# Kernel optimization log

Hardware: AMD Instinct MI355X
Metric: run time of the kernel (lower is better)

## Reference

```python
import jax, jax.numpy as jnp
import numpy as np

EPS = 1e-4
B, D, DOUT = 8192, 4096, 4096


def setup_inputs() -> dict:
    key = jax.random.key(0)
    k1, k2, k3 = jax.random.split(key, 3)
    x = jax.random.normal(k1, (B, D), dtype=jnp.float32)
    # Linear layer params (torch nn.Linear: y = x @ W.T + b)
    W = jax.random.normal(k2, (DOUT, D), dtype=jnp.float32) * (1.0 / np.sqrt(D))
    b = jax.random.normal(k3, (DOUT,), dtype=jnp.float32) * 0.01
    return {"x": x, "W": W, "b": b}


def reference(x, W, b):
    # hess = sum_b x[b] outer x[b] + eps*I  == X^T X + eps*I (a GEMM, not a
    # materialized [B,D,D] broadcast like the torch source)
    d = x.shape[1]
    hess = jnp.einsum('bi,bj->ij', x, x) + EPS * jnp.eye(d, dtype=x.dtype)
    out = x @ W.T + b  # wrapped nn.Linear
    return out, hess
```

## Files before the change

### kernel.cpp

```cpp
#include <hip/hip_runtime.h>
#include <hip/hip_bf16.h>

#define BDIM 8192
#define DDIM 4096
#define DOUTD 4096

typedef __attribute__((ext_vector_type(8))) short short8;
typedef __attribute__((ext_vector_type(16))) float floatx16;

__device__ inline unsigned short f32_to_bf16_rne(float f) {
    unsigned int u = __float_as_uint(f);
    unsigned int lsb = (u >> 16) & 1u;
    u += 0x7fffu + lsb;
    return (unsigned short)(u >> 16);
}

__device__ inline void gload_lds16(const void* g, void* lds) {
    __builtin_amdgcn_global_load_lds(
        (const __attribute__((address_space(1))) void*)g,
        (__attribute__((address_space(3))) void*)lds,
        16, 0, 0);
}

__global__ __launch_bounds__(256)
void convert_transpose_x(const float* __restrict__ x,
                         unsigned short* __restrict__ xb,
                         unsigned short* __restrict__ xT) {
    __shared__ __align__(8) unsigned short tile[64][66];
    const int t = threadIdx.x;
    const int tb = blockIdx.x * 64;
    const int td = blockIdx.y * 64;
#pragma unroll
    for (int p = 0; p < 4; ++p) {
        int c = t + p * 256;
        int row  = c >> 4;
        int col4 = (c & 15) << 2;
        float4 v = *(const float4*)&x[(size_t)(tb + row) * DDIM + td + col4];
        ushort4 o;
        o.x = f32_to_bf16_rne(v.x);
        o.y = f32_to_bf16_rne(v.y);
        o.z = f32_to_bf16_rne(v.z);
        o.w = f32_to_bf16_rne(v.w);
        *(ushort4*)&xb[(size_t)(tb + row) * DDIM + td + col4] = o;
        ushort2 lo; lo.x = o.x; lo.y = o.y;
        ushort2 hi2; hi2.x = o.z; hi2.y = o.w;
        *(ushort2*)&tile[row][col4]     = lo;
        *(ushort2*)&tile[row][col4 + 2] = hi2;
    }
    __syncthreads();
#pragma unroll
    for (int p = 0; p < 4; ++p) {
        int c = t + p * 256;
        int drow = c >> 4;
        int b4   = (c & 15) << 2;
        ushort4 o;
        o.x = tile[b4 + 0][drow];
        o.y = tile[b4 + 1][drow];
        o.z = tile[b4 + 2][drow];
        o.w = tile[b4 + 3][drow];
        *(ushort4*)&xT[(size_t)(td + drow) * BDIM + tb + b4] = o;
    }
}

__global__ __launch_bounds__(256)
void convert_w_kernel(const float* __restrict__ W, unsigned short* __restrict__ Wb) {
    size_t i = ((size_t)blockIdx.x * 256 + threadIdx.x) * 8;
    float4 a = *(const float4*)&W[i];
    float4 b = *(const float4*)&W[i + 4];
    short8 o;
    o[0] = (short)f32_to_bf16_rne(a.x);
    o[1] = (short)f32_to_bf16_rne(a.y);
    o[2] = (short)f32_to_bf16_rne(a.z);
    o[3] = (short)f32_to_bf16_rne(a.w);
    o[4] = (short)f32_to_bf16_rne(b.x);
    o[5] = (short)f32_to_bf16_rne(b.y);
    o[6] = (short)f32_to_bf16_rne(b.z);
    o[7] = (short)f32_to_bf16_rne(b.w);
    *(short8*)&Wb[i] = o;
}

#define CFENCE() asm volatile("" ::: "memory")
#define BAR() do { CFENCE(); __builtin_amdgcn_s_barrier(); CFENCE(); } while (0)
#define MFMA_BF16 __builtin_amdgcn_mfma_f32_32x32x16_bf16

template <bool HESS>
__global__ __launch_bounds__(512, 2)
void gemm256(const unsigned short* __restrict__ A,
             const unsigned short* __restrict__ B,
             const float* __restrict__ bias,
             float* __restrict__ C,
             int M, int N, int K) {
    __shared__ __align__(16) unsigned short As[32768];
    __shared__ __align__(16) unsigned short Bs[32768];

    const int t    = threadIdx.x;
    const int lane = t & 63;
    const int w    = t >> 6;
    const int lm   = lane & 31;
    const int hi   = lane >> 5;
    const int key2 = (lm >> 2) & 3;
    const int wm   = w >> 2;
    const int wn   = w & 3;
    const size_t bm = (size_t)blockIdx.y * 256;
    const size_t bn = (size_t)blockIdx.x * 256;
    const int NT = K >> 6;

    const int kh_w = w >> 2;
    const int wq   = w & 3;
    const int rsub = lane >> 2;
    const int csrc = (lane & 3) ^ ((lane >> 4) & 3);
    const unsigned short* gA0 = A + (bm + wq * 32 + rsub) * (size_t)K + kh_w * 32 + csrc * 8;
    const unsigned short* gB0 = B + (bn + wq * 32 + rsub) * (size_t)K + kh_w * 32 + csrc * 8;
    char* ldsA = (char*)As + kh_w * 16384 + wq * 2048;
    char* ldsB = (char*)Bs + kh_w * 16384 + wq * 2048;
    const size_t rowK16 = (size_t)16 * K;
    const size_t halfK  = (size_t)128 * K;

#define STAGE_A(tj, h, buf) do {                                   \
        const size_t _ko = (size_t)(tj) * 64 + (size_t)(h) * halfK;\
        char* _d = ldsA + (buf) * 32768 + (h) * 8192;              \
        gload_lds16(gA0 + _ko, _d);                                \
        gload_lds16(gA0 + _ko + rowK16, _d + 1024);                \
    } while (0)
#define STAGE_B(tj, h, buf) do {                                   \
        const size_t _ko = (size_t)(tj) * 64 + (size_t)(h) * halfK;\
        char* _d = ldsB + (buf) * 32768 + (h) * 8192;              \
        gload_lds16(gB0 + _ko, _d);                                \
        gload_lds16(gB0 + _ko + rowK16, _d + 1024);                \
    } while (0)

    const int AROWb = (wm * 128 + lm) * 32;
    const int BROWb = (wn * 32 + lm) * 32;
    int pos[4];
#pragma unroll
    for (int s = 0; s < 4; ++s)
        pos[s] = (s >> 1) * 8192 + ((((s & 1) * 2 + hi) ^ key2) * 8);

    floatx16 acc[4][2];
#pragma unroll
    for (int i = 0; i < 4; ++i)
#pragma unroll
        for (int j = 0; j < 2; ++j)
#pragma unroll
            for (int g = 0; g < 16; ++g)
                acc[i][j][g] = 0.f;

    short8 af0[2][4], af1[2][4], bf[2][4];

#define READS_EARLY(AB2) do {                                              \
        _Pragma("unroll")                                                  \
        for (int mi = 0; mi < 2; ++mi) {                                   \
            af0[mi][0] = *(const short8*)&As[(AB2) + AROWb + mi * 1024 + pos[0]]; \
            af0[mi][1] = *(const short8*)&As[(AB2) + AROWb + mi * 1024 + pos[1]]; \
        }                                                                  \
        bf[0][0] = *(const short8*)&Bs[(AB2) + BROWb + pos[0]];            \
        bf[0][1] = *(const short8*)&Bs[(AB2) + BROWb + pos[1]];            \
    } while (0)

#define TILE_BODY(J, BUFC) do {                                            \
        constexpr int AB  = (BUFC) * 16384;                                \
        constexpr int AB2 = ((BUFC) ^ 1) * 16384;                          \
         \
         \
        _Pragma("unroll")                                                  \
        for (int mi = 0; mi < 2; ++mi) {                                   \
            af0[mi][2] = *(const short8*)&As[AB + AROWb + mi * 1024 + pos[2]]; \
            af0[mi][3] = *(const short8*)&As[AB + AROWb + mi * 1024 + pos[3]]; \
        }                                                                  \
        bf[1][0] = *(const short8*)&Bs[AB + BROWb + 4096 + pos[0]];        \
        bf[1][1] = *(const short8*)&Bs[AB + BROWb + 4096 + pos[1]];        \
        if ((J) + 1 < NT) STAGE_B((J) + 1, 1, (BUFC) ^ 1);                 \
        BAR();                                                             \
        __builtin_amdgcn_s_setprio(1);                                     \
        _Pragma("unroll")                                                  \
        for (int s = 0; s < 2; ++s) {                                      \
            acc[0][0] = MFMA_BF16(af0[0][s], bf[0][s], acc[0][0], 0, 0, 0);\
            acc[1][0] = MFMA_BF16(af0[1][s], bf[0][s], acc[1][0], 0, 0, 0);\
            acc[0][1] = MFMA_BF16(af0[0][s], bf[1][s], acc[0][1], 0, 0, 0);\
            acc[1][1] = MFMA_BF16(af0[1][s], bf[1][s], acc[1][1], 0, 0, 0);\
        }                                                                  \
        __builtin_amdgcn_s_setprio(0);                                     \
        asm volatile("s_waitcnt lgkmcnt(0)" ::: "memory");                 \
        BAR();                                                             \
         \
         \
        bf[0][2] = *(const short8*)&Bs[AB + BROWb + pos[2]];               \
        bf[0][3] = *(const short8*)&Bs[AB + BROWb + pos[3]];               \
        bf[1][2] = *(const short8*)&Bs[AB + BROWb + 4096 + pos[2]];        \
        bf[1][3] = *(const short8*)&Bs[AB + BROWb + 4096 + pos[3]];        \
        _Pragma("unroll")                                                  \
        for (int mi = 0; mi < 2; ++mi) {                                   \
            af1[mi][0] = *(const short8*)&As[AB + AROWb + 2048 + mi * 1024 + pos[0]]; \
            af1[mi][1] = *(const short8*)&As[AB + AROWb + 2048 + mi * 1024 + pos[1]]; \
        }                                                                  \
        if ((J) + 2 < NT) STAGE_B((J) + 2, 0, (BUFC));                     \
        BAR();                                                             \
        __builtin_amdgcn_s_setprio(1);                                     \
        _Pragma("unroll")                                                  \
        for (int s = 2; s < 4; ++s) {                                      \
            acc[0][0] = MFMA_BF16(af0[0][s], bf[0][s], acc[0][0], 0, 0, 0);\
            acc[1][0] = MFMA_BF16(af0[1][s], bf[0][s], acc[1][0], 0, 0, 0);\
            acc[0][1] = MFMA_BF16(af0[0][s], bf[1][s], acc[0][1], 0, 0, 0);\
            acc[1][1] = MFMA_BF16(af0[1][s], bf[1][s], acc[1][1], 0, 0, 0);\
        }                                                                  \
        __builtin_amdgcn_s_setprio(0);                                     \
        asm volatile("s_waitcnt lgkmcnt(0)" ::: "memory");                 \
        BAR();                                                             \
         \
         \
        _Pragma("unroll")                                                  \
        for (int mi = 0; mi < 2; ++mi) {                                   \
            af1[mi][2] = *(const short8*)&As[AB + AROWb + 2048 + mi * 1024 + pos[2]]; \
            af1[mi][3] = *(const short8*)&As[AB + AROWb + 2048 + mi * 1024 + pos[3]]; \
        }                                                                  \
        if ((J) + 2 < NT) STAGE_A((J) + 2, 0, (BUFC));                     \
        BAR();                                                             \
        __builtin_amdgcn_s_setprio(1);                                     \
        _Pragma("unroll")                                                  \
        for (int s = 0; s < 2; ++s) {                                      \
            acc[2][0] = MFMA_BF16(af1[0][s], bf[0][s], acc[2][0], 0, 0, 0);\
            acc[3][0] = MFMA_BF16(af1[1][s], bf[0][s], acc[3][0], 0, 0, 0);\
            acc[2][1] = MFMA_BF16(af1[0][s], bf[1][s], acc[2][1], 0, 0, 0);\
            acc[3][1] = MFMA_BF16(af1[1][s], bf[1][s], acc[3][1], 0, 0, 0);\
        }                                                                  \
        __builtin_amdgcn_s_setprio(0);                                     \
        asm volatile("s_waitcnt lgkmcnt(0)" ::: "memory");                 \
        BAR();                                                             \
         \
         \
        if ((J) + 2 < NT) STAGE_A((J) + 2, 1, (BUFC));                     \
        if ((J) < NT - 2)       asm volatile("s_waitcnt vmcnt(6)" ::: "memory"); \
        else if ((J) == NT - 2) asm volatile("s_waitcnt vmcnt(0)" ::: "memory"); \
        BAR();                                                             \
        __builtin_amdgcn_s_setprio(1);                                     \
        _Pragma("unroll")                                                  \
        for (int s = 2; s < 4; ++s) {                                      \
            acc[2][0] = MFMA_BF16(af1[0][s], bf[0][s], acc[2][0], 0, 0, 0);\
            acc[3][0] = MFMA_BF16(af1[1][s], bf[0][s], acc[3][0], 0, 0, 0);\
            acc[2][1] = MFMA_BF16(af1[0][s], bf[1][s], acc[2][1], 0, 0, 0);\
            acc[3][1] = MFMA_BF16(af1[1][s], bf[1][s], acc[3][1], 0, 0, 0);\
        }                                                                  \
        __builtin_amdgcn_s_setprio(0);                                     \
        if ((J) + 1 < NT) READS_EARLY(AB2);                                \
        BAR();                                                             \
    } while (0)

    STAGE_B(0, 0, 0); STAGE_A(0, 0, 0); STAGE_B(0, 1, 0); STAGE_A(0, 1, 0);
    STAGE_B(1, 0, 1); STAGE_A(1, 0, 1); STAGE_A(1, 1, 1);
    asm volatile("s_waitcnt vmcnt(6)" ::: "memory");
    BAR();
    READS_EARLY(0);

    for (int jj = 0; jj < NT; jj += 2) {
        TILE_BODY(jj, 0);
        TILE_BODY(jj + 1, 1);
    }
#undef STAGE_A
#undef STAGE_B
#undef READS_EARLY
#undef TILE_BODY

    float bv[2];
#pragma unroll
    for (int n2 = 0; n2 < 2; ++n2)
        bv[n2] = HESS ? 0.f : bias[bn + n2 * 128 + wn * 32 + lm];
#pragma unroll
    for (int m4 = 0; m4 < 4; ++m4) {
        const size_t mbase = bm + wm * 128 + m4 * 32 + 4 * hi;
#pragma unroll
        for (int n2 = 0; n2 < 2; ++n2) {
            const size_t n = bn + n2 * 128 + wn * 32 + lm;
#pragma unroll
            for (int reg = 0; reg < 16; ++reg) {
                const size_t m = mbase + (reg & 3) + 8 * (reg >> 2);
                float v = acc[m4][n2][reg] + bv[n2];
                if (HESS && m == n) v += 1e-4f;
                C[m * N + n] = v;
            }
        }
    }
}

extern "C" void kernel_launch(void* const* d_in, const int* in_sizes, int n_in,
                              void* d_out, int out_size, void* d_ws, size_t ws_size,
                              hipStream_t stream) {
    const float* x = (const float*)d_in[0];
    const float* W = (const float*)d_in[1];
    const float* b = (const float*)d_in[2];

    float* out  = (float*)d_out;
    float* hess = out + (size_t)BDIM * DOUTD;

    unsigned short* xb = (unsigned short*)d_ws;
    unsigned short* xT = xb + (size_t)BDIM * DDIM;
    unsigned short* Wb = xT + (size_t)BDIM * DDIM;

    convert_transpose_x<<<dim3(BDIM / 64, DDIM / 64), 256, 0, stream>>>(x, xb, xT);
    convert_w_kernel<<<((size_t)DOUTD * DDIM) / 2048, 256, 0, stream>>>(W, Wb);

    gemm256<false><<<dim3(DOUTD / 256, BDIM / 256), 512, 0, stream>>>(
        xb, Wb, b, out, BDIM, DOUTD, DDIM);
    gemm256<true><<<dim3(DDIM / 256, DDIM / 256), 512, 0, stream>>>(
        xT, xT, nullptr, hess, DDIM, DDIM, BDIM);
}
```

Before: 885.7 us.

## Switch GEMM inner loop to 16x16x32 MFMA with reorganized fragment loads

Replaces the 32x32x16 bf16 MFMA with the 16x16x32 variant, re-indexing the accumulator into 8x4 tiles of 4-float fragments. The LDS fragment reads and the four-phase schedule inside each K tile are restructured: B fragments are reloaded per N half, A fragments per M half, and the separate early-read prefetch is removed. The epilogue mapping is updated to the 16x16 output layout. This trades the larger MFMA for more but smaller instructions and a different LDS read pattern, and may lose the earlier overlap of the next tile's reads with compute.

```diff
diff --git a/kernel.cpp b/kernel.cpp
--- a/kernel.cpp
+++ b/kernel.cpp
@@ -6,7 +6,7 @@
 #define DOUTD 4096
 
 typedef __attribute__((ext_vector_type(8))) short short8;
-typedef __attribute__((ext_vector_type(16))) float floatx16;
+typedef __attribute__((ext_vector_type(4))) float floatx4;
 
 __device__ inline unsigned short f32_to_bf16_rne(float f) {
     unsigned int u = __float_as_uint(f);
@@ -81,7 +81,7 @@
 
 #define CFENCE() asm volatile("" ::: "memory")
 #define BAR() do { CFENCE(); __builtin_amdgcn_s_barrier(); CFENCE(); } while (0)
-#define MFMA_BF16 __builtin_amdgcn_mfma_f32_32x32x16_bf16
+#define MFMA16 __builtin_amdgcn_mfma_f32_16x16x32_bf16
 
 template <bool HESS>
 __global__ __launch_bounds__(512, 2)
@@ -96,9 +96,8 @@
     const int t    = threadIdx.x;
     const int lane = t & 63;
     const int w    = t >> 6;
-    const int lm   = lane & 31;
-    const int hi   = lane >> 5;
-    const int key2 = (lm >> 2) & 3;
+    const int l15  = lane & 15;
+    const int lq   = lane >> 4;
     const int wm   = w >> 2;
     const int wn   = w & 3;
     const size_t bm = (size_t)blockIdx.y * 256;
@@ -129,127 +128,106 @@
         gload_lds16(gB0 + _ko + rowK16, _d + 1024);                \
     } while (0)
 
-    const int AROWb = (wm * 128 + lm) * 32;
-    const int BROWb = (wn * 32 + lm) * 32;
-    int pos[4];
-#pragma unroll
-    for (int s = 0; s < 4; ++s)
-        pos[s] = (s >> 1) * 8192 + ((((s & 1) * 2 + hi) ^ key2) * 8);
-
-    floatx16 acc[4][2];
-#pragma unroll
-    for (int i = 0; i < 4; ++i)
-#pragma unroll
-        for (int j = 0; j < 2; ++j)
-#pragma unroll
-            for (int g = 0; g < 16; ++g)
+    const int pofs  = ((lq ^ ((l15 >> 2) & 3)) << 3);
+    const int AROW0 = (wm * 128 + l15) * 32 + pofs;
+    const int BROW0 = (wn * 32 + l15) * 32 + pofs;
+
+    floatx4 acc[8][4];
+#pragma unroll
+    for (int i = 0; i < 8; ++i)
+#pragma unroll
+        for (int j = 0; j < 4; ++j)
+#pragma unroll
+            for (int g = 0; g < 4; ++g)
                 acc[i][j][g] = 0.f;
 
-    short8 af0[2][4], af1[2][4], bf[2][4];
-
-#define READS_EARLY(AB2) do {                                              \
-        _Pragma("unroll")                                                  \
-        for (int mi = 0; mi < 2; ++mi) {                                   \
-            af0[mi][0] = *(const short8*)&As[(AB2) + AROWb + mi * 1024 + pos[0]]; \
-            af0[mi][1] = *(const short8*)&As[(AB2) + AROWb + mi * 1024 + pos[1]]; \
-        }                                                                  \
-        bf[0][0] = *(const short8*)&Bs[(AB2) + BROWb + pos[0]];            \
-        bf[0][1] = *(const short8*)&Bs[(AB2) + BROWb + pos[1]];            \
-    } while (0)
+    short8 af0[4][2], af1[4][2], bfr[2][2];
 
 #define TILE_BODY(J, BUFC) do {                                            \
-        constexpr int AB  = (BUFC) * 16384;                                \
-        constexpr int AB2 = ((BUFC) ^ 1) * 16384;                          \
-         \
-         \
-        _Pragma("unroll")                                                  \
-        for (int mi = 0; mi < 2; ++mi) {                                   \
-            af0[mi][2] = *(const short8*)&As[AB + AROWb + mi * 1024 + pos[2]]; \
-            af0[mi][3] = *(const short8*)&As[AB + AROWb + mi * 1024 + pos[3]]; \
-        }                                                                  \
-        bf[1][0] = *(const short8*)&Bs[AB + BROWb + 4096 + pos[0]];        \
-        bf[1][1] = *(const short8*)&Bs[AB + BROWb + 4096 + pos[1]];        \
+        constexpr int AB = (BUFC) * 16384;                                 \
+             \
+        _Pragma("unroll")                                                  \
+        for (int nf = 0; nf < 2; ++nf)                                     \
+            _Pragma("unroll")                                              \
+            for (int ks = 0; ks < 2; ++ks)                                 \
+                bfr[nf][ks] = *(const short8*)&Bs[AB + ks * 8192 + BROW0 + nf * 512]; \
+        _Pragma("unroll")                                                  \
+        for (int mf = 0; mf < 4; ++mf)                                     \
+            _Pragma("unroll")                                              \
+            for (int ks = 0; ks < 2; ++ks)                                 \
+                af0[mf][ks] = *(const short8*)&As[AB + ks * 8192 + AROW0 + mf * 512]; \
         if ((J) + 1 < NT) STAGE_B((J) + 1, 1, (BUFC) ^ 1);                 \
         BAR();                                                             \
         __builtin_amdgcn_s_setprio(1);                                     \
         _Pragma("unroll")                                                  \
-        for (int s = 0; s < 2; ++s) {                                      \
-            acc[0][0] = MFMA_BF16(af0[0][s], bf[0][s], acc[0][0], 0, 0, 0);\
-            acc[1][0] = MFMA_BF16(af0[1][s], bf[0][s], acc[1][0], 0, 0, 0);\
-            acc[0][1] = MFMA_BF16(af0[0][s], bf[1][s], acc[0][1], 0, 0, 0);\
-            acc[1][1] = MFMA_BF16(af0[1][s], bf[1][s], acc[1][1], 0, 0, 0);\
-        }                                                                  \
+        for (int ks = 0; ks < 2; ++ks)                                     \
+            _Pragma("unroll")                                              \
+            for (int nf = 0; nf < 2; ++nf)                                 \
+                _Pragma("unroll")                                          \
+                for (int mf = 0; mf < 4; ++mf)                             \
+                    acc[mf][nf] = MFMA16(af0[mf][ks], bfr[nf][ks], acc[mf][nf], 0, 0, 0); \
         __builtin_amdgcn_s_setprio(0);                                     \
         asm volatile("s_waitcnt lgkmcnt(0)" ::: "memory");                 \
         BAR();                                                             \
-         \
-         \
-        bf[0][2] = *(const short8*)&Bs[AB + BROWb + pos[2]];               \
-        bf[0][3] = *(const short8*)&Bs[AB + BROWb + pos[3]];               \
-        bf[1][2] = *(const short8*)&Bs[AB + BROWb + 4096 + pos[2]];        \
-        bf[1][3] = *(const short8*)&Bs[AB + BROWb + 4096 + pos[3]];        \
-        _Pragma("unroll")                                                  \
-        for (int mi = 0; mi < 2; ++mi) {                                   \
-            af1[mi][0] = *(const short8*)&As[AB + AROWb + 2048 + mi * 1024 + pos[0]]; \
-            af1[mi][1] = *(const short8*)&As[AB + AROWb + 2048 + mi * 1024 + pos[1]]; \
-        }                                                                  \
+                        \
+        _Pragma("unroll")                                                  \
+        for (int mf = 0; mf < 4; ++mf)                                     \
+            _Pragma("unroll")                                              \
+            for (int ks = 0; ks < 2; ++ks)                                 \
+                af1[mf][ks] = *(const short8*)&As[AB + ks * 8192 + AROW0 + (4 + mf) * 512]; \
         if ((J) + 2 < NT) STAGE_B((J) + 2, 0, (BUFC));                     \
         BAR();                                                             \
         __builtin_amdgcn_s_setprio(1);                                     \
         _Pragma("unroll")                                                  \
-        for (int s = 2; s < 4; ++s) {                                      \
-            acc[0][0] = MFMA_BF16(af0[0][s], bf[0][s], acc[0][0], 0, 0, 0);\
-            acc[1][0] = MFMA_BF16(af0[1][s], bf[0][s], acc[1][0], 0, 0, 0);\
-            acc[0][1] = MFMA_BF16(af0[0][s], bf[1][s], acc[0][1], 0, 0, 0);\
-            acc[1][1] = MFMA_BF16(af0[1][s], bf[1][s], acc[1][1], 0, 0, 0);\
-        }                                                                  \
+        for (int ks = 0; ks < 2; ++ks)                                     \
+            _Pragma("unroll")                                              \
+            for (int nf = 0; nf < 2; ++nf)                                 \
+                _Pragma("unroll")                                          \
+                for (int mf = 0; mf < 4; ++mf)                             \
+                    acc[4 + mf][nf] = MFMA16(af1[mf][ks], bfr[nf][ks], acc[4 + mf][nf], 0, 0, 0); \
         __builtin_amdgcn_s_setprio(0);                                     \
         asm volatile("s_waitcnt lgkmcnt(0)" ::: "memory");                 \
         BAR();                                                             \
-         \
-         \
-        _Pragma("unroll")                                                  \
-        for (int mi = 0; mi < 2; ++mi) {                                   \
-            af1[mi][2] = *(const short8*)&As[AB + AROWb + 2048 + mi * 1024 + pos[2]]; \
-            af1[mi][3] = *(const short8*)&As[AB + AROWb + 2048 + mi * 1024 + pos[3]]; \
-        }                                                                  \
+                           \
+        _Pragma("unroll")                                                  \
+        for (int nf = 0; nf < 2; ++nf)                                     \
+            _Pragma("unroll")                                              \
+            for (int ks = 0; ks < 2; ++ks)                                 \
+                bfr[nf][ks] = *(const short8*)&Bs[AB + ks * 8192 + BROW0 + 4096 + nf * 512]; \
         if ((J) + 2 < NT) STAGE_A((J) + 2, 0, (BUFC));                     \
         BAR();                                                             \
         __builtin_amdgcn_s_setprio(1);                                     \
         _Pragma("unroll")                                                  \
-        for (int s = 0; s < 2; ++s) {                                      \
-            acc[2][0] = MFMA_BF16(af1[0][s], bf[0][s], acc[2][0], 0, 0, 0);\
-            acc[3][0] = MFMA_BF16(af1[1][s], bf[0][s], acc[3][0], 0, 0, 0);\
-            acc[2][1] = MFMA_BF16(af1[0][s], bf[1][s], acc[2][1], 0, 0, 0);\
-            acc[3][1] = MFMA_BF16(af1[1][s], bf[1][s], acc[3][1], 0, 0, 0);\
-        }                                                                  \
+        for (int ks = 0; ks < 2; ++ks)                                     \
+            _Pragma("unroll")                                              \
+            for (int nf = 0; nf < 2; ++nf)                                 \
+                _Pragma("unroll")                                          \
+                for (int mf = 0; mf < 4; ++mf)                             \
+                    acc[4 + mf][2 + nf] = MFMA16(af1[mf][ks], bfr[nf][ks], acc[4 + mf][2 + nf], 0, 0, 0); \
         __builtin_amdgcn_s_setprio(0);                                     \
         asm volatile("s_waitcnt lgkmcnt(0)" ::: "memory");                 \
         BAR();                                                             \
-         \
          \
         if ((J) + 2 < NT) STAGE_A((J) + 2, 1, (BUFC));                     \
+        BAR();                                                             \
+        __builtin_amdgcn_s_setprio(1);                                     \
+        _Pragma("unroll")                                                  \
+        for (int ks = 0; ks < 2; ++ks)                                     \
+            _Pragma("unroll")                                              \
+            for (int nf = 0; nf < 2; ++nf)                                 \
+                _Pragma("unroll")                                          \
+                for (int mf = 0; mf < 4; ++mf)                             \
+                    acc[mf][2 + nf] = MFMA16(af0[mf][ks], bfr[nf][ks], acc[mf][2 + nf], 0, 0, 0); \
+        __builtin_amdgcn_s_setprio(0);                                     \
         if ((J) < NT - 2)       asm volatile("s_waitcnt vmcnt(6)" ::: "memory"); \
         else if ((J) == NT - 2) asm volatile("s_waitcnt vmcnt(0)" ::: "memory"); \
         BAR();                                                             \
-        __builtin_amdgcn_s_setprio(1);                                     \
-        _Pragma("unroll")                                                  \
-        for (int s = 2; s < 4; ++s) {                                      \
-            acc[2][0] = MFMA_BF16(af1[0][s], bf[0][s], acc[2][0], 0, 0, 0);\
-            acc[3][0] = MFMA_BF16(af1[1][s], bf[0][s], acc[3][0], 0, 0, 0);\
-            acc[2][1] = MFMA_BF16(af1[0][s], bf[1][s], acc[2][1], 0, 0, 0);\
-            acc[3][1] = MFMA_BF16(af1[1][s], bf[1][s], acc[3][1], 0, 0, 0);\
-        }                                                                  \
-        __builtin_amdgcn_s_setprio(0);                                     \
-        if ((J) + 1 < NT) READS_EARLY(AB2);                                \
-        BAR();                                                             \
     } while (0)
 
-    STAGE_B(0, 0, 0); STAGE_A(0, 0, 0); STAGE_B(0, 1, 0); STAGE_A(0, 1, 0);
+    STAGE_B(0, 0, 0); STAGE_A(0, 0, 0); STAGE_A(0, 1, 0); STAGE_B(0, 1, 0);
     STAGE_B(1, 0, 1); STAGE_A(1, 0, 1); STAGE_A(1, 1, 1);
     asm volatile("s_waitcnt vmcnt(6)" ::: "memory");
     BAR();
-    READS_EARLY(0);
 
     for (int jj = 0; jj < NT; jj += 2) {
         TILE_BODY(jj, 0);
@@ -257,23 +235,22 @@
     }
 #undef STAGE_A
 #undef STAGE_B
-#undef READS_EARLY
 #undef TILE_BODY
 
-    float bv[2];
-#pragma unroll
-    for (int n2 = 0; n2 < 2; ++n2)
-        bv[n2] = HESS ? 0.f : bias[bn + n2 * 128 + wn * 32 + lm];
-#pragma unroll
-    for (int m4 = 0; m4 < 4; ++m4) {
-        const size_t mbase = bm + wm * 128 + m4 * 32 + 4 * hi;
-#pragma unroll
-        for (int n2 = 0; n2 < 2; ++n2) {
-            const size_t n = bn + n2 * 128 + wn * 32 + lm;
-#pragma unroll
-            for (int reg = 0; reg < 16; ++reg) {
-                const size_t m = mbase + (reg & 3) + 8 * (reg >> 2);
-                float v = acc[m4][n2][reg] + bv[n2];
+    float bv[4];
+#pragma unroll
+    for (int q = 0; q < 4; ++q)
+        bv[q] = HESS ? 0.f : bias[bn + (q >> 1) * 128 + wn * 32 + (q & 1) * 16 + l15];
+#pragma unroll
+    for (int mf = 0; mf < 8; ++mf) {
+        const size_t mbase = bm + wm * 128 + mf * 16 + lq * 4;
+#pragma unroll
+        for (int q = 0; q < 4; ++q) {
+            const size_t n = bn + (q >> 1) * 128 + wn * 32 + (q & 1) * 16 + l15;
+#pragma unroll
+            for (int reg = 0; reg < 4; ++reg) {
+                const size_t m = mbase + reg;
+                float v = acc[mf][q][reg] + bv[q];
                 if (HESS && m == n) v += 1e-4f;
                 C[m * N + n] = v;
             }
```

New measurement: 900.6 us. Within noise of the previous version (+1.7%).
